# Performance work log

Measured on AMD Instinct MI355X. Metric: run time of the kernel, lower is better.

Reference implementation:

```python
import jax, jax.numpy as jnp
import numpy as np

N, E = 50000, 800000
IN, HID, OUT, H = 128, 32, 32, 4
NEG_SLOPE = 0.2
EPS = 1e-5


def layernorm(x, g, b):
    mu = x.mean(-1, keepdims=True)
    var = ((x - mu) ** 2).mean(-1, keepdims=True)
    return (x - mu) * jax.lax.rsqrt(var + EPS) * g + b


def gat_conv(x, src, dst, W, a_s, a_d, bias, heads, ch, concat):
    n = x.shape[0]
    h = (x @ W).reshape(n, heads, ch)               # [N,H,C]
    alpha_s = (h * a_s).sum(-1)                     # [N,H]
    alpha_d = (h * a_d).sum(-1)                     # [N,H]
    e = jax.nn.leaky_relu(alpha_s[src] + alpha_d[dst], NEG_SLOPE)  # [E,H]
    m = jax.ops.segment_max(e, dst, num_segments=n)
    m = jnp.where(jnp.isfinite(m), m, 0.0)
    ex = jnp.exp(e - m[dst])
    denom = jax.ops.segment_sum(ex, dst, num_segments=n)
    alpha = ex / (denom[dst] + 1e-16)               # [E,H]
    msg = h[src] * alpha[:, :, None]                # [E,H,C]
    out = jax.ops.segment_sum(msg, dst, num_segments=n)  # [N,H,C]
    out = out.reshape(n, heads * ch) if concat else out.mean(axis=1)
    return out + bias


def setup_inputs() -> dict:
    key = jax.random.key(0)
    ks = jax.random.split(key, 24)
    HC = HID * H
    s = 0.05
    inp = {
        "x": jax.random.normal(ks[0], (N, IN), jnp.float32),
        "edge_index": jax.random.randint(ks[1], (2, E), 0, N),
        "W1": jax.random.normal(ks[2], (IN, HC), jnp.float32) * s,
        "as1": jax.random.normal(ks[3], (H, HID), jnp.float32) * s,
        "ad1": jax.random.normal(ks[4], (H, HID), jnp.float32) * s,
        "b1": jnp.zeros((HC,), jnp.float32),
        "g1": jnp.ones((HC,), jnp.float32),
        "be1": jnp.zeros((HC,), jnp.float32),
        "W2": jax.random.normal(ks[5], (HC, HC), jnp.float32) * s,
        "as2": jax.random.normal(ks[6], (H, HID), jnp.float32) * s,
        "ad2": jax.random.normal(ks[7], (H, HID), jnp.float32) * s,
        "b2": jnp.zeros((HC,), jnp.float32),
        "g2": jnp.ones((HC,), jnp.float32),
        "be2": jnp.zeros((HC,), jnp.float32),
        "W3": jax.random.normal(ks[8], (HC, OUT * H), jnp.float32) * s,
        "as3": jax.random.normal(ks[9], (H, OUT), jnp.float32) * s,
        "ad3": jax.random.normal(ks[10], (H, OUT), jnp.float32) * s,
        "b3": jnp.zeros((OUT,), jnp.float32),
        "Wsk": jax.random.normal(ks[11], (IN, HC), jnp.float32) * s,
        "bsk": jnp.zeros((HC,), jnp.float32),
    }
    return inp


def reference(x, edge_index, W1, as1, ad1, b1, g1, be1, W2, as2, ad2, b2, g2, be2, W3, as3, ad3, b3, Wsk, bsk):
    n = x.shape[0]
    loops = jnp.arange(n, dtype=edge_index.dtype)
    src = jnp.concatenate([edge_index[0], loops])
    dst = jnp.concatenate([edge_index[1], loops])
    h = gat_conv(x, src, dst, W1, as1, ad1, b1, H, HID, True)
    h = jax.nn.elu(h)
    h = layernorm(h, g1, be1)
    h = h + (x @ Wsk + bsk)  # residual (dropout is identity in eval)
    h = gat_conv(h, src, dst, W2, as2, ad2, b2, H, HID, True)
    h = jax.nn.elu(h)
    h = layernorm(h, g2, be2)
    h = gat_conv(h, src, dst, W3, as3, ad3, b3, H, OUT, False)
    return h
```

## Files before the change

### kernel.cpp

```cpp
#include <hip/hip_runtime.h>
#include <hip/hip_bf16.h>

typedef __attribute__((ext_vector_type(8))) short short8;
typedef __attribute__((ext_vector_type(4))) float f32x4;
using bf16 = __hip_bfloat16;

#define NEG_SLOPE 0.2f
#define LN_EPS 1e-5f

__device__ __forceinline__ unsigned short f2bfu(float v) {
    bf16 t = __float2bfloat16(v);
    unsigned short s;
    __builtin_memcpy(&s, &t, 2);
    return s;
}
__device__ __forceinline__ short f2bf(float v) {
    bf16 t = __float2bfloat16(v);
    short s;
    __builtin_memcpy(&s, &t, 2);
    return s;
}
__device__ __forceinline__ unsigned packbf(float a, float b) {
    return (unsigned)f2bfu(a) | ((unsigned)f2bfu(b) << 16);
}
__device__ __forceinline__ float bflo(unsigned u) { return __uint_as_float(u << 16); }
__device__ __forceinline__ float bfhi(unsigned u) { return __uint_as_float(u & 0xffff0000u); }
__device__ __forceinline__ float bf1(unsigned short u) { return __uint_as_float(((unsigned)u) << 16); }

__global__ void detect_k(const void* __restrict__ x, int* flag,
                         int* bucketCur, int CAP) {
    int lane = threadIdx.x;
    for (int i = lane; i < 512; i += 64) bucketCur[i] = i * CAP;
    const unsigned short* u = (const unsigned short*)x;
    float m = 0.f;
    for (int i = lane; i < 8192; i += 64) {
        float v = fabsf(bf1(u[i]));
        if (!(v == v)) v = 1e30f;
        m = fmaxf(m, v);
    }
    for (int d = 1; d < 64; d <<= 1) m = fmaxf(m, __shfl_xor(m, d));
    if (lane == 0) flag[0] = (m > 1e4f) ? 1 : 0;
}

struct Ptr4 { const void* p[4]; };
struct Ptr14 { const void* p[14]; };
struct Ptr3 { const void* p[3]; };
struct Ptr6 { const void* p[6]; };
__global__ void stage_k(Ptr4 Ws, bf16* __restrict__ WT,
                        Ptr14 ptrs, bf16* __restrict__ sv,
                        Ptr3 Wv, Ptr6 av, bf16* __restrict__ vaT,
                        const int* __restrict__ flag) {
    int b = blockIdx.x;
    int f = flag[0];
    if (b < 256) {
        int gid = b * 256 + threadIdx.x;
        int m = gid >> 14;
        int idx = gid & 16383;
        int i = idx >> 7, j = idx & 127;
        const void* W = Ws.p[m];
        float v = f ? ((const float*)W)[idx]
                    : __bfloat162float(((const bf16*)W)[idx]);
        WT[m * 16384 + j * 128 + i] = __float2bfloat16(v);
    } else if (b == 256) {
        for (int k = threadIdx.x; k < 14 * 128; k += 256) {
            int t = k >> 7, i = k & 127;
            int n = (t == 12) ? 32 : 128;
            if (i < n) {
                const void* s = ptrs.p[t];
                float v = f ? ((const float*)s)[i]
                            : __bfloat162float(((const bf16*)s)[i]);
                sv[k] = __float2bfloat16(v);
            }
        }
    } else {
        int gid = (b - 257) * 256 + threadIdx.x;
        int l = gid >> 11;
        if (l >= 3) return;
        int c = (gid >> 7) & 15, k = gid & 127;
        float acc = 0.f;
        if (c < 8) {
            int hd = c & 3;
            const void* W = Wv.p[l];
            const void* a = av.p[l * 2 + (c >> 2)];
            for (int j = 0; j < 32; ++j) {
                float wv = f ? ((const float*)W)[k * 128 + hd * 32 + j]
                             : __bfloat162float(((const bf16*)W)[k * 128 + hd * 32 + j]);
                float avv = f ? ((const float*)a)[hd * 32 + j]
                              : __bfloat162float(((const bf16*)a)[hd * 32 + j]);
                acc += wv * avv;
            }
        }
        vaT[gid] = __float2bfloat16(acc);
    }
}

#define SCAT_EPB 2048
__global__ __launch_bounds__(256) void bscatter_k(const int* __restrict__ src,
                                                  const int* __restrict__ dst,
                                                  int* bucketCur,
                                                  int* __restrict__ ebuf,
                                                  int E, int NB, int CAP) {
    __shared__ int lcnt[512], lbase[512];
    int t = threadIdx.x;
    int e0 = blockIdx.x * SCAT_EPB;
    int cnt = E - e0;
    if (cnt > SCAT_EPB) cnt = SCAT_EPB;
    for (int i = t; i < NB; i += 256) lcnt[i] = 0;
    __syncthreads();
    for (int i = t; i < cnt; i += 256)
        atomicAdd(&lcnt[dst[e0 + i] >> 7], 1);
    __syncthreads();
    for (int i = t; i < NB; i += 256) {
        int c = lcnt[i];
        lbase[i] = c ? atomicAdd(&bucketCur[i], c) : 0;
        lcnt[i] = 0;
    }
    __syncthreads();
    for (int i = t; i < cnt; i += 256) {
        int d = dst[e0 + i];
        int b = d >> 7;
        int pos = lbase[b] + atomicAdd(&lcnt[b], 1);
        if (pos < (b + 1) * CAP)
            ebuf[pos] = ((d & 127) << 16) | src[e0 + i];
    }
}

__global__ __launch_bounds__(256) void build_k(const int* __restrict__ ebuf,
                                               const int* __restrict__ bucketCur,
                                               int* __restrict__ rowSE,
                                               int* __restrict__ colSrc,
                                               int N, int CAP) {
    int b = blockIdx.x, t = threadIdx.x;
    int base = b * CAP;
    int cnt = bucketCur[b] - base;
    if (cnt > CAP) cnt = CAP;
    __shared__ int nodeCnt[128], nodeCur[128], ws2[2];
    if (t < 128) nodeCnt[t] = 0;
    __syncthreads();
    for (int i = t; i < cnt; i += 256)
        atomicAdd(&nodeCnt[ebuf[base + i] >> 16], 1);
    __syncthreads();
    int v = 0, incl = 0;
    if (t < 128) {
        v = nodeCnt[t];
        incl = v;
        for (int d = 1; d < 64; d <<= 1) {
            int u = __shfl_up(incl, d);
            if ((t & 63) >= d) incl += u;
        }
        if ((t & 63) == 63) ws2[t >> 6] = incl;
    }
    __syncthreads();
    if (t < 128) {
        int excl = incl - v + ((t >= 64) ? ws2[0] : 0);
        int node = b * 128 + t;
        if (node < N) {
            rowSE[node * 2] = base + excl;
            rowSE[node * 2 + 1] = base + excl + v;
        }
        nodeCur[t] = excl;
    }
    __syncthreads();
    for (int i = t; i < cnt; i += 256) {
        int p = ebuf[base + i];
        int pos = base + atomicAdd(&nodeCur[p >> 16], 1);
        colSrc[pos] = (p & 0xffff) << 8;
    }
    for (int i = cnt + t; i < CAP; i += 256)
        colSrc[base + i] = 0;
}

template <int DUAL>
__global__ __launch_bounds__(256) void gemm_k(const void* __restrict__ A,
                                              const bf16* __restrict__ WT,
                                              bf16* __restrict__ out0,
                                              bf16* __restrict__ out1,
                                              const bf16* __restrict__ bias1,
                                              const bf16* __restrict__ vaT,
                                              float* __restrict__ asN,
                                              float* __restrict__ adN,
                                              int N, const int* __restrict__ flag) {
    int wave = threadIdx.x >> 6, lane = threadIdx.x & 63;
    int lm = lane & 15, lk = lane >> 4;
    const short* Ws = (const short*)WT;
    const short* Vs = (const short*)vaT;
    bool f32m = flag && flag[0];

    short8 bw0[2][4], bw1[DUAL ? 2 : 1][DUAL ? 4 : 1];
#pragma unroll
    for (int ct = 0; ct < 2; ++ct) {
        int c = (wave * 2 + ct) * 16 + lm;
#pragma unroll
        for (int kk = 0; kk < 4; ++kk)
            bw0[ct][kk] = *(const short8*)(Ws + (size_t)c * 128 + kk * 32 + lk * 8);
    }
    if (DUAL) {
#pragma unroll
        for (int ct = 0; ct < 2; ++ct) {
            int c = (wave * 2 + ct) * 16 + lm;
#pragma unroll
            for (int kk = 0; kk < 4; ++kk)
                bw1[ct][kk] = *(const short8*)(Ws + 16384 + (size_t)c * 128 + kk * 32 + lk * 8);
        }
    }
    short8 va8[4];
    if (wave == 0) {
#pragma unroll
        for (int kk = 0; kk < 4; ++kk)
            va8[kk] = *(const short8*)(Vs + (size_t)lm * 128 + kk * 32 + lk * 8);
    }
    float bv[DUAL ? 2 : 1];
    if (DUAL) {
#pragma unroll
        for (int ct = 0; ct < 2; ++ct)
            bv[ct] = __bfloat162float(bias1[(wave * 2 + ct) * 16 + lm]);
    }

    int stride = gridDim.x * 32;
    for (int rowBase = blockIdx.x * 32; rowBase < N; rowBase += stride) {
        short8 af[2][4];
#pragma unroll
        for (int rt = 0; rt < 2; ++rt) {
            int r = rowBase + rt * 16 + lm;
            if (r >= N) r = N - 1;
            if (f32m) {
#pragma unroll
                for (int kk = 0; kk < 4; ++kk) {
                    const float* Af = (const float*)A + (size_t)r * 128 + kk * 32 + lk * 8;
                    float4 q0 = *(const float4*)(Af);
                    float4 q1 = *(const float4*)(Af + 4);
                    short8 v;
                    v[0] = f2bf(q0.x); v[1] = f2bf(q0.y); v[2] = f2bf(q0.z); v[3] = f2bf(q0.w);
                    v[4] = f2bf(q1.x); v[5] = f2bf(q1.y); v[6] = f2bf(q1.z); v[7] = f2bf(q1.w);
                    af[rt][kk] = v;
                }
            } else {
#pragma unroll
                for (int kk = 0; kk < 4; ++kk)
                    af[rt][kk] = *(const short8*)((const short*)A + (size_t)r * 128 + kk * 32 + lk * 8);
            }
        }

        f32x4 acc0[2][2];
        f32x4 acc1[DUAL ? 2 : 1][DUAL ? 2 : 1];
#pragma unroll
        for (int ct = 0; ct < 2; ++ct)
#pragma unroll
            for (int rt = 0; rt < 2; ++rt) acc0[ct][rt] = (f32x4){0.f, 0.f, 0.f, 0.f};
        if (DUAL) {
#pragma unroll
            for (int ct = 0; ct < 2; ++ct)
#pragma unroll
                for (int rt = 0; rt < 2; ++rt) acc1[ct][rt] = (f32x4){0.f, 0.f, 0.f, 0.f};
        }

#pragma unroll
        for (int rt = 0; rt < 2; ++rt) {
#pragma unroll
            for (int kk = 0; kk < 4; ++kk) {
                acc0[0][rt] = __builtin_amdgcn_mfma_f32_16x16x32_bf16(af[rt][kk], bw0[0][kk], acc0[0][rt], 0, 0, 0);
                acc0[1][rt] = __builtin_amdgcn_mfma_f32_16x16x32_bf16(af[rt][kk], bw0[1][kk], acc0[1][rt], 0, 0, 0);
                if (DUAL) {
                    acc1[0][rt] = __builtin_amdgcn_mfma_f32_16x16x32_bf16(af[rt][kk], bw1[0][kk], acc1[0][rt], 0, 0, 0);
                    acc1[1][rt] = __builtin_amdgcn_mfma_f32_16x16x32_bf16(af[rt][kk], bw1[1][kk], acc1[1][rt], 0, 0, 0);
                }
            }
        }

#pragma unroll
        for (int ct = 0; ct < 2; ++ct) {
            int c = (wave * 2 + ct) * 16 + lm;
#pragma unroll
            for (int rt = 0; rt < 2; ++rt) {
#pragma unroll
                for (int i = 0; i < 4; ++i) {
                    int r = rowBase + rt * 16 + lk * 4 + i;
                    if (r < N) out0[(size_t)r * 128 + c] = __float2bfloat16(acc0[ct][rt][i]);
                }
            }
        }
        if (DUAL) {
#pragma unroll
            for (int ct = 0; ct < 2; ++ct) {
                int c = (wave * 2 + ct) * 16 + lm;
#pragma unroll
                for (int rt = 0; rt < 2; ++rt) {
#pragma unroll
                    for (int i = 0; i < 4; ++i) {
                        int r = rowBase + rt * 16 + lk * 4 + i;
                        if (r < N) out1[(size_t)r * 128 + c] = __float2bfloat16(acc1[ct][rt][i] + bv[ct]);
                    }
                }
            }
        }

        if (wave == 0) {
            f32x4 accA[2];
#pragma unroll
            for (int rt = 0; rt < 2; ++rt) accA[rt] = (f32x4){0.f, 0.f, 0.f, 0.f};
#pragma unroll
            for (int rt = 0; rt < 2; ++rt)
#pragma unroll
                for (int kk = 0; kk < 4; ++kk)
                    accA[rt] = __builtin_amdgcn_mfma_f32_16x16x32_bf16(af[rt][kk], va8[kk], accA[rt], 0, 0, 0);
            if (lm < 8) {
                float* dst = (lm < 4) ? asN : adN;
                int hh = lm & 3;
#pragma unroll
                for (int rt = 0; rt < 2; ++rt)
#pragma unroll
                    for (int i = 0; i < 4; ++i) {
                        int r = rowBase + rt * 16 + lk * 4 + i;
                        if (r < N) dst[(size_t)r * 4 + hh] = accA[rt][i];
                    }
            }
        }
    }
}

template <int MODE>
__global__ __launch_bounds__(256) void agg_k(const bf16* __restrict__ h,
                                             const float* __restrict__ asN,
                                             const float* __restrict__ adN,
                                             const int* __restrict__ rowSE,
                                             const int* __restrict__ colSrc,
                                             const bf16* __restrict__ bvec,
                                             const bf16* __restrict__ g,
                                             const bf16* __restrict__ be,
                                             void* outv, int N,
                                             const int* __restrict__ flag) {
    int wv = threadIdx.x >> 6, lane = threadIdx.x & 63;
    int n = blockIdx.x * 4 + wv;
    if (n >= N) return;
    int grp = lane >> 4, t = lane & 15;
    int hd = t >> 2;
    const char* hbase = (const char*)h + t * 16;
    const char* abase = (const char*)asN + hd * 4;

    int2 se = ((const int2*)rowSE)[n];
    int st = se.x, en = se.y;
    if (en < st) en = st;

    uint4 hself = *(const uint4*)(hbase + (size_t)n * 256);
    float adn = adN[(size_t)n * 4 + hd];
    float asn_self = asN[(size_t)n * 4 + hd];

    float a[8];
#pragma unroll
    for (int k = 0; k < 8; ++k) a[k] = 0.f;
    float den = 0.f;

    int j = st + grp;
    int off = (j < en) ? colSrc[j] : 0;
    float av = *(const float*)(abase + (off >> 4));
    uint4 hq = *(const uint4*)(hbase + off);
    for (; j < en; j += 4) {
        int off2 = colSrc[j + 4];
        float av2 = *(const float*)(abase + (off2 >> 4));
        uint4 hq2 = *(const uint4*)(hbase + off2);
        float e = av + adn;
        float w = __expf(fmaxf(e, NEG_SLOPE * e));
        den += w;
        a[0] += w * bflo(hq.x); a[1] += w * bfhi(hq.x);
        a[2] += w * bflo(hq.y); a[3] += w * bfhi(hq.y);
        a[4] += w * bflo(hq.z); a[5] += w * bfhi(hq.z);
        a[6] += w * bflo(hq.w); a[7] += w * bfhi(hq.w);
        av = av2; hq = hq2;
    }

#pragma unroll
    for (int k = 0; k < 8; ++k) {
        a[k] += __shfl_xor(a[k], 16);
        a[k] += __shfl_xor(a[k], 32);
    }
    den += __shfl_xor(den, 16);
    den += __shfl_xor(den, 32);

    float es = asn_self + adn;
    float wsf = __expf(fmaxf(es, NEG_SLOPE * es));
    den += wsf;
    a[0] += wsf * bflo(hself.x); a[1] += wsf * bfhi(hself.x);
    a[2] += wsf * bflo(hself.y); a[3] += wsf * bfhi(hself.y);
    a[4] += wsf * bflo(hself.z); a[5] += wsf * bfhi(hself.z);
    a[6] += wsf * bflo(hself.w); a[7] += wsf * bfhi(hself.w);

    float inv = 1.f / (den + 1e-16f);
    float y[8];
#pragma unroll
    for (int k = 0; k < 8; ++k) y[k] = a[k] * inv;

    if (MODE == 3) {
#pragma unroll
        for (int k = 0; k < 8; ++k) {
            y[k] += __shfl_xor(y[k], 4);
            y[k] += __shfl_xor(y[k], 8);
            y[k] *= 0.25f;
        }
        if (lane < 4) {
            int u = lane;
            uint4 bp = *(const uint4*)((const unsigned short*)bvec + u * 8);
            float v0 = y[0] + bflo(bp.x), v1 = y[1] + bfhi(bp.x);
            float v2 = y[2] + bflo(bp.y), v3 = y[3] + bfhi(bp.y);
            float v4 = y[4] + bflo(bp.z), v5 = y[5] + bfhi(bp.z);
            float v6 = y[6] + bflo(bp.w), v7 = y[7] + bfhi(bp.w);
            if (flag[0]) {
                float4* op = (float4*)outv + (size_t)n * 8 + u * 2;
                op[0] = make_float4(v0, v1, v2, v3);
                op[1] = make_float4(v4, v5, v6, v7);
            } else {
                uint4 pk;
                pk.x = packbf(v0, v1); pk.y = packbf(v2, v3);
                pk.z = packbf(v4, v5); pk.w = packbf(v6, v7);
                ((uint4*)outv)[(size_t)n * 4 + u] = pk;
            }
        }
    } else {
        unsigned short* out = (unsigned short*)outv;
        uint4 bp = *(const uint4*)((const unsigned short*)bvec + t * 8);
        y[0] += bflo(bp.x); y[1] += bfhi(bp.x);
        y[2] += bflo(bp.y); y[3] += bfhi(bp.y);
        y[4] += bflo(bp.z); y[5] += bfhi(bp.z);
        y[6] += bflo(bp.w); y[7] += bfhi(bp.w);
#pragma unroll
        for (int k = 0; k < 8; ++k) y[k] = y[k] > 0.f ? y[k] : (__expf(y[k]) - 1.f);
        float s = 0.f, q = 0.f;
#pragma unroll
        for (int k = 0; k < 8; ++k) { s += y[k]; q += y[k] * y[k]; }
        for (int d = 1; d < 16; d <<= 1) {
            s += __shfl_xor(s, d);
            q += __shfl_xor(q, d);
        }
        float mu = s * (1.f / 128.f);
        float var = q * (1.f / 128.f) - mu * mu;
        var = fmaxf(var, 0.f);
        float rs = rsqrtf(var + LN_EPS);
        if (lane < 16) {
            uint4 gp = *(const uint4*)((const unsigned short*)g + t * 8);
            uint4 ep = *(const uint4*)((const unsigned short*)be + t * 8);
            float z[8];
            z[0] = (y[0] - mu) * rs * bflo(gp.x) + bflo(ep.x);
            z[1] = (y[1] - mu) * rs * bfhi(gp.x) + bfhi(ep.x);
            z[2] = (y[2] - mu) * rs * bflo(gp.y) + bflo(ep.y);
            z[3] = (y[3] - mu) * rs * bfhi(gp.y) + bfhi(ep.y);
            z[4] = (y[4] - mu) * rs * bflo(gp.z) + bflo(ep.z);
            z[5] = (y[5] - mu) * rs * bfhi(gp.z) + bfhi(ep.z);
            z[6] = (y[6] - mu) * rs * bflo(gp.w) + bflo(ep.w);
            z[7] = (y[7] - mu) * rs * bfhi(gp.w) + bfhi(ep.w);
            if (MODE == 1) {
                uint4 sk = *(uint4*)(out + (size_t)n * 128 + t * 8);
                z[0] += bflo(sk.x); z[1] += bfhi(sk.x);
                z[2] += bflo(sk.y); z[3] += bfhi(sk.y);
                z[4] += bflo(sk.z); z[5] += bfhi(sk.z);
                z[6] += bflo(sk.w); z[7] += bfhi(sk.w);
            }
            uint4 pk;
            pk.x = packbf(z[0], z[1]); pk.y = packbf(z[2], z[3]);
            pk.z = packbf(z[4], z[5]); pk.w = packbf(z[6], z[7]);
            *(uint4*)(out + (size_t)n * 128 + t * 8) = pk;
        }
    }
}

extern "C" void kernel_launch(void* const* d_in, const int* in_sizes, int n_in,
                              void* d_out, int out_size, void* d_ws, size_t ws_size,
                              hipStream_t stream) {
    const void* x  = d_in[0];
    const int*  ei = (const int*)d_in[1];

    int N = in_sizes[0] / 128;
    int E = in_sizes[1] / 2;
    const int* srcI = ei;
    const int* dstI = ei + E;

    int NB = (N + 127) >> 7;
    int CAP = (E / NB + 1024 + 511) & ~511;

    char* w = (char*)d_ws;
    size_t o = 0;
    auto carve = [&](size_t bytes) {
        void* p = w + o;
        o += (bytes + 255) & ~(size_t)255;
        return p;
    };
    int*  dtFlag = (int*)carve(256);
    bf16* WTall = (bf16*)carve(4 * 16384 * 2);
    bf16* sv   = (bf16*)carve(14 * 128 * 2);
    bf16* vaT  = (bf16*)carve(3 * 16 * 128 * 2);
    bf16* hB   = (bf16*)carve((size_t)N * 128 * 2);
    bf16* xB   = (bf16*)carve((size_t)N * 128 * 2);
    float* asN = (float*)carve((size_t)N * 4 * 4);
    float* adN = (float*)carve((size_t)N * 4 * 4);
    int* rowSE = (int*)carve((size_t)N * 2 * 4);
    int* colSrc= (int*)carve((size_t)NB * CAP * 4 + 64);
    int* ebuf  = (int*)carve((size_t)NB * CAP * 4);
    int* bucketCur = (int*)carve(512 * 4);

    detect_k<<<1, 64, 0, stream>>>(x, dtFlag, bucketCur, CAP);

    Ptr4 wp;
    wp.p[0] = d_in[2];  wp.p[1] = d_in[18];
    wp.p[2] = d_in[8];  wp.p[3] = d_in[14];
    Ptr14 ptrs;
    ptrs.p[0] = d_in[3];  ptrs.p[1] = d_in[4];  ptrs.p[2] = d_in[5];
    ptrs.p[3] = d_in[6];  ptrs.p[4] = d_in[7];
    ptrs.p[5] = d_in[9];  ptrs.p[6] = d_in[10]; ptrs.p[7] = d_in[11];
    ptrs.p[8] = d_in[12]; ptrs.p[9] = d_in[13];
    ptrs.p[10] = d_in[15]; ptrs.p[11] = d_in[16]; ptrs.p[12] = d_in[17];
    ptrs.p[13] = d_in[19];
    Ptr3 wv3;
    wv3.p[0] = d_in[2]; wv3.p[1] = d_in[8]; wv3.p[2] = d_in[14];
    Ptr6 av6;
    av6.p[0] = d_in[3];  av6.p[1] = d_in[4];
    av6.p[2] = d_in[9];  av6.p[3] = d_in[10];
    av6.p[4] = d_in[15]; av6.p[5] = d_in[16];

    stage_k<<<281, 256, 0, stream>>>(wp, WTall, ptrs, sv, wv3, av6, vaT, dtFlag);

    bscatter_k<<<(E + SCAT_EPB - 1) / SCAT_EPB, 256, 0, stream>>>(srcI, dstI,
                                                                 bucketCur, ebuf, E, NB, CAP);
    build_k<<<NB, 256, 0, stream>>>(ebuf, bucketCur, rowSE, colSrc, N, CAP);

    int gb = (N + 63) / 64;
    int nb4 = (N + 3) / 4;

    gemm_k<1><<<gb, 256, 0, stream>>>(x, WTall, hB, xB, sv + 13 * 128,
                                      vaT, asN, adN, N, dtFlag);
    agg_k<1><<<nb4, 256, 0, stream>>>(hB, asN, adN, rowSE, colSrc,
                                      sv + 2 * 128, sv + 3 * 128, sv + 4 * 128,
                                      xB, N, dtFlag);

    gemm_k<0><<<gb, 256, 0, stream>>>(xB, WTall + 2 * 16384, hB, nullptr, nullptr,
                                      vaT + 2048, asN, adN, N, nullptr);
    agg_k<2><<<nb4, 256, 0, stream>>>(hB, asN, adN, rowSE, colSrc,
                                      sv + 7 * 128, sv + 8 * 128, sv + 9 * 128,
                                      xB, N, dtFlag);

    gemm_k<0><<<gb, 256, 0, stream>>>(xB, WTall + 3 * 16384, hB, nullptr, nullptr,
                                      vaT + 4096, asN, adN, N, nullptr);
    agg_k<3><<<nb4, 256, 0, stream>>>(hB, asN, adN, rowSE, colSrc,
                                      sv + 12 * 128, nullptr, nullptr,
                                      d_out, N, dtFlag);
}
```

Measured before the change: 349.7 us.

## Fuse aggregation epilogue with next layer's GEMM and attention projections

Merges each layer-1/2 aggregation kernel with the following layer's feature GEMM and attention-coefficient MFMA. Each block aggregates 16 nodes into LDS, then multiplies the tile by the next weight matrix, so the normalized activations never go to global memory. Ping-pong buffers avoid read/write hazards between layers. The cost is a 16-node block whose waves each process 4 nodes serially before a block barrier, which may reduce latency hiding in the gather loop.

```diff
diff --git a/kernel.cpp b/kernel.cpp
--- a/kernel.cpp
+++ b/kernel.cpp
@@ -319,16 +319,193 @@
 }
 
 template <int MODE>
-__global__ __launch_bounds__(256) void agg_k(const bf16* __restrict__ h,
-                                             const float* __restrict__ asN,
-                                             const float* __restrict__ adN,
-                                             const int* __restrict__ rowSE,
-                                             const int* __restrict__ colSrc,
-                                             const bf16* __restrict__ bvec,
-                                             const bf16* __restrict__ g,
-                                             const bf16* __restrict__ be,
-                                             void* outv, int N,
-                                             const int* __restrict__ flag) {
+__global__ __launch_bounds__(256) void aggemm_k(const bf16* __restrict__ h,
+                                                const float* __restrict__ asN,
+                                                const float* __restrict__ adN,
+                                                const int* __restrict__ rowSE,
+                                                const int* __restrict__ colSrc,
+                                                const bf16* __restrict__ bvec,
+                                                const bf16* __restrict__ g,
+                                                const bf16* __restrict__ be,
+                                                const bf16* __restrict__ WT,
+                                                const bf16* __restrict__ vaT,
+                                                bf16* hOut,
+                                                float* __restrict__ asOut,
+                                                float* __restrict__ adOut, int N) {
+    __shared__ unsigned short zs[16 * 136];
+    int wv = threadIdx.x >> 6, lane = threadIdx.x & 63;
+    int grp = lane >> 4, t = lane & 15;
+    int hd = t >> 2;
+    int blockBase = blockIdx.x * 16;
+    const char* hbase = (const char*)h + t * 16;
+    const char* abase = (const char*)asN + hd * 4;
+
+    for (int q = 0; q < 4; ++q) {
+        int n = blockBase + wv * 4 + q;
+        uint4 zpk = make_uint4(0, 0, 0, 0);
+        if (n < N) {
+            int2 se = ((const int2*)rowSE)[n];
+            int st = se.x, en = se.y;
+            if (en < st) en = st;
+
+            uint4 hself = *(const uint4*)(hbase + (size_t)n * 256);
+            float adn = adN[(size_t)n * 4 + hd];
+            float asn_self = asN[(size_t)n * 4 + hd];
+
+            float a[8];
+#pragma unroll
+            for (int k = 0; k < 8; ++k) a[k] = 0.f;
+            float den = 0.f;
+
+            int j = st + grp;
+            int off = (j < en) ? colSrc[j] : 0;
+            float av = *(const float*)(abase + (off >> 4));
+            uint4 hq = *(const uint4*)(hbase + off);
+            for (; j < en; j += 4) {
+                int off2 = colSrc[j + 4];
+                float av2 = *(const float*)(abase + (off2 >> 4));
+                uint4 hq2 = *(const uint4*)(hbase + off2);
+                float e = av + adn;
+                float w = __expf(fmaxf(e, NEG_SLOPE * e));
+                den += w;
+                a[0] += w * bflo(hq.x); a[1] += w * bfhi(hq.x);
+                a[2] += w * bflo(hq.y); a[3] += w * bfhi(hq.y);
+                a[4] += w * bflo(hq.z); a[5] += w * bfhi(hq.z);
+                a[6] += w * bflo(hq.w); a[7] += w * bfhi(hq.w);
+                av = av2; hq = hq2;
+            }
+
+#pragma unroll
+            for (int k = 0; k < 8; ++k) {
+                a[k] += __shfl_xor(a[k], 16);
+                a[k] += __shfl_xor(a[k], 32);
+            }
+            den += __shfl_xor(den, 16);
+            den += __shfl_xor(den, 32);
+
+            float es = asn_self + adn;
+            float wsf = __expf(fmaxf(es, NEG_SLOPE * es));
+            den += wsf;
+            a[0] += wsf * bflo(hself.x); a[1] += wsf * bfhi(hself.x);
+            a[2] += wsf * bflo(hself.y); a[3] += wsf * bfhi(hself.y);
+            a[4] += wsf * bflo(hself.z); a[5] += wsf * bfhi(hself.z);
+            a[6] += wsf * bflo(hself.w); a[7] += wsf * bfhi(hself.w);
+
+            float inv = 1.f / (den + 1e-16f);
+            float y[8];
+#pragma unroll
+            for (int k = 0; k < 8; ++k) y[k] = a[k] * inv;
+
+            uint4 bp = *(const uint4*)((const unsigned short*)bvec + t * 8);
+            y[0] += bflo(bp.x); y[1] += bfhi(bp.x);
+            y[2] += bflo(bp.y); y[3] += bfhi(bp.y);
+            y[4] += bflo(bp.z); y[5] += bfhi(bp.z);
+            y[6] += bflo(bp.w); y[7] += bfhi(bp.w);
+#pragma unroll
+            for (int k = 0; k < 8; ++k) y[k] = y[k] > 0.f ? y[k] : (__expf(y[k]) - 1.f);
+            float s = 0.f, qq = 0.f;
+#pragma unroll
+            for (int k = 0; k < 8; ++k) { s += y[k]; qq += y[k] * y[k]; }
+            for (int d = 1; d < 16; d <<= 1) {
+                s += __shfl_xor(s, d);
+                qq += __shfl_xor(qq, d);
+            }
+            float mu = s * (1.f / 128.f);
+            float var = qq * (1.f / 128.f) - mu * mu;
+            var = fmaxf(var, 0.f);
+            float rs = rsqrtf(var + LN_EPS);
+            if (lane < 16) {
+                uint4 gp = *(const uint4*)((const unsigned short*)g + t * 8);
+                uint4 ep = *(const uint4*)((const unsigned short*)be + t * 8);
+                float z[8];
+                z[0] = (y[0] - mu) * rs * bflo(gp.x) + bflo(ep.x);
+                z[1] = (y[1] - mu) * rs * bfhi(gp.x) + bfhi(ep.x);
+                z[2] = (y[2] - mu) * rs * bflo(gp.y) + bflo(ep.y);
+                z[3] = (y[3] - mu) * rs * bfhi(gp.y) + bfhi(ep.y);
+                z[4] = (y[4] - mu) * rs * bflo(gp.z) + bflo(ep.z);
+                z[5] = (y[5] - mu) * rs * bfhi(gp.z) + bfhi(ep.z);
+                z[6] = (y[6] - mu) * rs * bflo(gp.w) + bflo(ep.w);
+                z[7] = (y[7] - mu) * rs * bfhi(gp.w) + bfhi(ep.w);
+                if (MODE == 1) {
+                    uint4 sk = *(uint4*)((unsigned short*)hOut + (size_t)n * 128 + t * 8);
+                    z[0] += bflo(sk.x); z[1] += bfhi(sk.x);
+                    z[2] += bflo(sk.y); z[3] += bfhi(sk.y);
+                    z[4] += bflo(sk.z); z[5] += bfhi(sk.z);
+                    z[6] += bflo(sk.w); z[7] += bfhi(sk.w);
+                }
+                zpk.x = packbf(z[0], z[1]); zpk.y = packbf(z[2], z[3]);
+                zpk.z = packbf(z[4], z[5]); zpk.w = packbf(z[6], z[7]);
+            }
+        }
+        if (lane < 16)
+            *(uint4*)((char*)zs + (wv * 4 + q) * 272 + t * 16) = zpk;
+    }
+    __syncthreads();
+
+    int lm = t, lk = grp;
+    const short* Ws = (const short*)WT;
+    short8 af[4];
+#pragma unroll
+    for (int kk = 0; kk < 4; ++kk)
+        af[kk] = *(const short8*)((const char*)zs + lm * 272 + kk * 64 + lk * 16);
+
+    short8 bw[2][4];
+#pragma unroll
+    for (int ct = 0; ct < 2; ++ct) {
+        int c = (wv * 2 + ct) * 16 + lm;
+#pragma unroll
+        for (int kk = 0; kk < 4; ++kk)
+            bw[ct][kk] = *(const short8*)(Ws + (size_t)c * 128 + kk * 32 + lk * 8);
+    }
+
+    f32x4 acc[2];
+    acc[0] = (f32x4){0.f, 0.f, 0.f, 0.f};
+    acc[1] = (f32x4){0.f, 0.f, 0.f, 0.f};
+#pragma unroll
+    for (int kk = 0; kk < 4; ++kk) {
+        acc[0] = __builtin_amdgcn_mfma_f32_16x16x32_bf16(af[kk], bw[0][kk], acc[0], 0, 0, 0);
+        acc[1] = __builtin_amdgcn_mfma_f32_16x16x32_bf16(af[kk], bw[1][kk], acc[1], 0, 0, 0);
+    }
+#pragma unroll
+    for (int ct = 0; ct < 2; ++ct) {
+        int c = (wv * 2 + ct) * 16 + lm;
+#pragma unroll
+        for (int i = 0; i < 4; ++i) {
+            int r = blockBase + lk * 4 + i;
+            if (r < N) hOut[(size_t)r * 128 + c] = __float2bfloat16(acc[ct][i]);
+        }
+    }
+
+    if (wv == 0) {
+        const short* Vs = (const short*)vaT;
+        short8 va8[4];
+#pragma unroll
+        for (int kk = 0; kk < 4; ++kk)
+            va8[kk] = *(const short8*)(Vs + (size_t)lm * 128 + kk * 32 + lk * 8);
+        f32x4 accA = (f32x4){0.f, 0.f, 0.f, 0.f};
+#pragma unroll
+        for (int kk = 0; kk < 4; ++kk)
+            accA = __builtin_amdgcn_mfma_f32_16x16x32_bf16(af[kk], va8[kk], accA, 0, 0, 0);
+        if (lm < 8) {
+            float* dst = (lm < 4) ? asOut : adOut;
+            int hh = lm & 3;
+#pragma unroll
+            for (int i = 0; i < 4; ++i) {
+                int r = blockBase + lk * 4 + i;
+                if (r < N) dst[(size_t)r * 4 + hh] = accA[i];
+            }
+        }
+    }
+}
+
+__global__ __launch_bounds__(256) void agg3_k(const bf16* __restrict__ h,
+                                              const float* __restrict__ asN,
+                                              const float* __restrict__ adN,
+                                              const int* __restrict__ rowSE,
+                                              const int* __restrict__ colSrc,
+                                              const bf16* __restrict__ bvec,
+                                              void* outv, int N,
+                                              const int* __restrict__ flag) {
     int wv = threadIdx.x >> 6, lane = threadIdx.x & 63;
     int n = blockIdx.x * 4 + wv;
     if (n >= N) return;
@@ -389,74 +566,28 @@
 #pragma unroll
     for (int k = 0; k < 8; ++k) y[k] = a[k] * inv;
 
-    if (MODE == 3) {
-#pragma unroll
-        for (int k = 0; k < 8; ++k) {
-            y[k] += __shfl_xor(y[k], 4);
-            y[k] += __shfl_xor(y[k], 8);
-            y[k] *= 0.25f;
-        }
-        if (lane < 4) {
-            int u = lane;
-            uint4 bp = *(const uint4*)((const unsigned short*)bvec + u * 8);
-            float v0 = y[0] + bflo(bp.x), v1 = y[1] + bfhi(bp.x);
-            float v2 = y[2] + bflo(bp.y), v3 = y[3] + bfhi(bp.y);
-            float v4 = y[4] + bflo(bp.z), v5 = y[5] + bfhi(bp.z);
-            float v6 = y[6] + bflo(bp.w), v7 = y[7] + bfhi(bp.w);
-            if (flag[0]) {
-                float4* op = (float4*)outv + (size_t)n * 8 + u * 2;
-                op[0] = make_float4(v0, v1, v2, v3);
-                op[1] = make_float4(v4, v5, v6, v7);
-            } else {
-                uint4 pk;
-                pk.x = packbf(v0, v1); pk.y = packbf(v2, v3);
-                pk.z = packbf(v4, v5); pk.w = packbf(v6, v7);
-                ((uint4*)outv)[(size_t)n * 4 + u] = pk;
-            }
-        }
-    } else {
-        unsigned short* out = (unsigned short*)outv;
-        uint4 bp = *(const uint4*)((const unsigned short*)bvec + t * 8);
-        y[0] += bflo(bp.x); y[1] += bfhi(bp.x);
-        y[2] += bflo(bp.y); y[3] += bfhi(bp.y);
-        y[4] += bflo(bp.z); y[5] += bfhi(bp.z);
-        y[6] += bflo(bp.w); y[7] += bfhi(bp.w);
-#pragma unroll
-        for (int k = 0; k < 8; ++k) y[k] = y[k] > 0.f ? y[k] : (__expf(y[k]) - 1.f);
-        float s = 0.f, q = 0.f;
-#pragma unroll
-        for (int k = 0; k < 8; ++k) { s += y[k]; q += y[k] * y[k]; }
-        for (int d = 1; d < 16; d <<= 1) {
-            s += __shfl_xor(s, d);
-            q += __shfl_xor(q, d);
-        }
-        float mu = s * (1.f / 128.f);
-        float var = q * (1.f / 128.f) - mu * mu;
-        var = fmaxf(var, 0.f);
-        float rs = rsqrtf(var + LN_EPS);
-        if (lane < 16) {
-            uint4 gp = *(const uint4*)((const unsigned short*)g + t * 8);
-            uint4 ep = *(const uint4*)((const unsigned short*)be + t * 8);
-            float z[8];
-            z[0] = (y[0] - mu) * rs * bflo(gp.x) + bflo(ep.x);
-            z[1] = (y[1] - mu) * rs * bfhi(gp.x) + bfhi(ep.x);
-            z[2] = (y[2] - mu) * rs * bflo(gp.y) + bflo(ep.y);
-            z[3] = (y[3] - mu) * rs * bfhi(gp.y) + bfhi(ep.y);
-            z[4] = (y[4] - mu) * rs * bflo(gp.z) + bflo(ep.z);
-            z[5] = (y[5] - mu) * rs * bfhi(gp.z) + bfhi(ep.z);
-            z[6] = (y[6] - mu) * rs * bflo(gp.w) + bflo(ep.w);
-            z[7] = (y[7] - mu) * rs * bfhi(gp.w) + bfhi(ep.w);
-            if (MODE == 1) {
-                uint4 sk = *(uint4*)(out + (size_t)n * 128 + t * 8);
-                z[0] += bflo(sk.x); z[1] += bfhi(sk.x);
-                z[2] += bflo(sk.y); z[3] += bfhi(sk.y);
-                z[4] += bflo(sk.z); z[5] += bfhi(sk.z);
-                z[6] += bflo(sk.w); z[7] += bfhi(sk.w);
-            }
+#pragma unroll
+    for (int k = 0; k < 8; ++k) {
+        y[k] += __shfl_xor(y[k], 4);
+        y[k] += __shfl_xor(y[k], 8);
+        y[k] *= 0.25f;
+    }
+    if (lane < 4) {
+        int u = lane;
+        uint4 bp = *(const uint4*)((const unsigned short*)bvec + u * 8);
+        float v0 = y[0] + bflo(bp.x), v1 = y[1] + bfhi(bp.x);
+        float v2 = y[2] + bflo(bp.y), v3 = y[3] + bfhi(bp.y);
+        float v4 = y[4] + bflo(bp.z), v5 = y[5] + bfhi(bp.z);
+        float v6 = y[6] + bflo(bp.w), v7 = y[7] + bfhi(bp.w);
+        if (flag[0]) {
+            float4* op = (float4*)outv + (size_t)n * 8 + u * 2;
+            op[0] = make_float4(v0, v1, v2, v3);
+            op[1] = make_float4(v4, v5, v6, v7);
+        } else {
             uint4 pk;
-            pk.x = packbf(z[0], z[1]); pk.y = packbf(z[2], z[3]);
-            pk.z = packbf(z[4], z[5]); pk.w = packbf(z[6], z[7]);
-            *(uint4*)(out + (size_t)n * 128 + t * 8) = pk;
+            pk.x = packbf(v0, v1); pk.y = packbf(v2, v3);
+            pk.z = packbf(v4, v5); pk.w = packbf(v6, v7);
+            ((uint4*)outv)[(size_t)n * 4 + u] = pk;
         }
     }
 }
@@ -486,10 +617,12 @@
     bf16* WTall = (bf16*)carve(4 * 16384 * 2);
     bf16* sv   = (bf16*)carve(14 * 128 * 2);
     bf16* vaT  = (bf16*)carve(3 * 16 * 128 * 2);
-    bf16* hB   = (bf16*)carve((size_t)N * 128 * 2);
-    bf16* xB   = (bf16*)carve((size_t)N * 128 * 2);
-    float* asN = (float*)carve((size_t)N * 4 * 4);
-    float* adN = (float*)carve((size_t)N * 4 * 4);
+    bf16* bufP = (bf16*)carve((size_t)N * 128 * 2);
+    bf16* bufQ = (bf16*)carve((size_t)N * 128 * 2);
+    float* asA = (float*)carve((size_t)N * 4 * 4);
+    float* adA = (float*)carve((size_t)N * 4 * 4);
+    float* asB = (float*)carve((size_t)N * 4 * 4);
+    float* adB = (float*)carve((size_t)N * 4 * 4);
     int* rowSE = (int*)carve((size_t)N * 2 * 4);
     int* colSrc= (int*)carve((size_t)NB * CAP * 4 + 64);
     int* ebuf  = (int*)carve((size_t)NB * CAP * 4);
@@ -521,23 +654,19 @@
     build_k<<<NB, 256, 0, stream>>>(ebuf, bucketCur, rowSE, colSrc, N, CAP);
 
     int gb = (N + 63) / 64;
+    int nbF = (N + 15) / 16;
     int nb4 = (N + 3) / 4;
 
-    gemm_k<1><<<gb, 256, 0, stream>>>(x, WTall, hB, xB, sv + 13 * 128,
-                                      vaT, asN, adN, N, dtFlag);
-    agg_k<1><<<nb4, 256, 0, stream>>>(hB, asN, adN, rowSE, colSrc,
-                                      sv + 2 * 128, sv + 3 * 128, sv + 4 * 128,
-                                      xB, N, dtFlag);
-
-    gemm_k<0><<<gb, 256, 0, stream>>>(xB, WTall + 2 * 16384, hB, nullptr, nullptr,
-                                      vaT + 2048, asN, adN, N, nullptr);
-    agg_k<2><<<nb4, 256, 0, stream>>>(hB, asN, adN, rowSE, colSrc,
-                                      sv + 7 * 128, sv + 8 * 128, sv + 9 * 128,
-                                      xB, N, dtFlag);
-
-    gemm_k<0><<<gb, 256, 0, stream>>>(xB, WTall + 3 * 16384, hB, nullptr, nullptr,
-                                      vaT + 4096, asN, adN, N, nullptr);
-    agg_k<3><<<nb4, 256, 0, stream>>>(hB, asN, adN, rowSE, colSrc,
-                                      sv + 12 * 128, nullptr, nullptr,
-                                      d_out, N, dtFlag);
-}
+    gemm_k<1><<<gb, 256, 0, stream>>>(x, WTall, bufP, bufQ, sv + 13 * 128,
+                                      vaT, asA, adA, N, dtFlag);
+    aggemm_k<1><<<nbF, 256, 0, stream>>>(bufP, asA, adA, rowSE, colSrc,
+                                         sv + 2 * 128, sv + 3 * 128, sv + 4 * 128,
+                                         WTall + 2 * 16384, vaT + 2048,
+                                         bufQ, asB, adB, N);
+    aggemm_k<2><<<nbF, 256, 0, stream>>>(bufQ, asB, adB, rowSE, colSrc,
+                                         sv + 7 * 128, sv + 8 * 128, sv + 9 * 128,
+                                         WTall + 3 * 16384, vaT + 4096,
+                                         bufP, asA, adA, N);
+    agg3_k<<<nb4, 256, 0, stream>>>(bufP, asA, adA, rowSE, colSrc,
+                                    sv + 12 * 128, d_out, N, dtFlag);
+}
```

New measurement: 350.4 us. About the same (+0.2%).
